# Performance work log

Hardware: AMD Instinct MI355X
Metric: run time of the kernel (lower is better)

## Reference

```python
import jax, jax.numpy as jnp
import numpy as np

B, T, C, H = 4, 4096, 1024, 64

def setup_inputs() -> dict:
    key = jax.random.key(0)
    k1, k2, k3, k4 = jax.random.split(key, 4)
    x = jax.random.normal(k1, (B, T, C), dtype=jnp.float32)
    # nn.Linear(C, H, bias=False): y = x @ W^T with W [H, C]; store as [C, H] for x @ W
    Wq = jax.random.normal(k2, (C, H), dtype=jnp.float32) * (C ** -0.5)
    Wk = jax.random.normal(k3, (C, H), dtype=jnp.float32) * (C ** -0.5)
    Wv = jax.random.normal(k4, (C, H), dtype=jnp.float32) * (C ** -0.5)
    return {"x": x, "Wq": Wq, "Wk": Wk, "Wv": Wv}

def reference(x, Wq, Wk, Wv):
    # Manual causal single-head attention (dropout p=0 -> identity).
    q = x @ Wq  # [B, T, H]
    k = x @ Wk  # [B, T, H]
    v = x @ Wv  # [B, T, H]
    scale = q.shape[-1] ** -0.5
    w = jnp.einsum('bth,bsh->bts', q, k) * scale  # [B, T, T] scores
    causal = jnp.tril(jnp.ones((x.shape[1], x.shape[1]), dtype=bool))
    w = jnp.where(causal, w, -jnp.inf)
    w = jax.nn.softmax(w, axis=-1)
    out = jnp.einsum('bts,bsh->bth', w, v)  # [B, T, H]
    return out
```

## Files before the change

### kernel.cpp

```cpp
#include <hip/hip_runtime.h>
#include <math.h>

#define Bn 4
#define Tn 4096
#define Cn 1024
#define Hn 64

typedef __attribute__((ext_vector_type(8))) short short8;
typedef __attribute__((ext_vector_type(4))) float floatx4;
typedef unsigned short ushort_t;

#define QSCALE 0.1803368801111204f

__device__ __forceinline__ ushort_t f2bf(float f) {
  union { float f; unsigned u; } v; v.f = f;
  unsigned r = v.u + 0x7FFFu + ((v.u >> 16) & 1u);
  return (ushort_t)(r >> 16);
}
__device__ __forceinline__ ushort_t f2bf_hu(float f) {
  union { float f; unsigned u; } v; v.f = f;
  return (ushort_t)((v.u + 0x8000u) >> 16);
}
__device__ __forceinline__ float bf2f(ushort_t h) {
  union { unsigned u; float f; } v; v.u = ((unsigned)h) << 16; return v.f;
}


__global__ __launch_bounds__(256) void wf_kernel(
    const float* __restrict__ Wq, const float* __restrict__ Wk,
    const float* __restrict__ Wv, ushort_t* __restrict__ Wf)
{
  __shared__ float ws[32][65];
  const int tid = threadIdx.x;
  const int m = blockIdx.x >> 5;
  const int g = blockIdx.x & 31;
  const float* W = (m == 0) ? Wq : (m == 1) ? Wk : Wv;
  const float4* src = (const float4*)(W + (size_t)g * 32 * Hn);
#pragma unroll
  for (int it = 0; it < 2; ++it) {
    int i4 = it * 256 + tid;
    float4 v = src[i4];
    int c = i4 >> 4, h = (i4 & 15) * 4;
    ws[c][h] = v.x; ws[c][h + 1] = v.y; ws[c][h + 2] = v.z; ws[c][h + 3] = v.w;
  }
  __syncthreads();
  const int nt = tid >> 6, lane = tid & 63;
  const int col = lane & 15, quad = lane >> 4;
  ushort_t t[8];
#pragma unroll
  for (int e = 0; e < 8; ++e) t[e] = f2bf(ws[quad * 8 + e][nt * 16 + col]);
  *(short8*)(Wf + ((size_t)((m * 32 + g) * 4 + nt) * 64 + lane) * 8) = *(short8*)t;
}

__global__ __launch_bounds__(256, 2) void qkv_proj_kernel(
    const float* __restrict__ x, const ushort_t* __restrict__ Wf,
    ushort_t* __restrict__ Qf, ushort_t* __restrict__ Kf,
    ushort_t* __restrict__ Vf)
{
  __shared__ __align__(16) char smem[67584];
  ushort_t* xs  = (ushort_t*)smem;
  ushort_t* red = (ushort_t*)smem;
  ushort_t* img = (ushort_t*)(smem + 49152);

  const int tid  = threadIdx.x;
  const int wv   = tid >> 6;
  const int lane = tid & 63;
  const int col  = lane & 15;
  const int quad = lane >> 4;
  const int blk  = blockIdx.x;
  const int row0 = blk * 32;

#pragma unroll
  for (int jj = 0; jj < 32; ++jj) {
    float4 v = *(const float4*)(x + (size_t)(row0 + jj) * Cn + wv * 256 + lane * 4);
    ushort4 u;
    u.x = f2bf(v.x); u.y = f2bf(v.y); u.z = f2bf(v.z); u.w = f2bf(v.w);
    *(ushort4*)(xs + (wv * 32 + jj) * 264 + lane * 4) = u;
  }

  floatx4 acc[2][3][4];
#pragma unroll
  for (int sub = 0; sub < 2; ++sub)
#pragma unroll
    for (int m = 0; m < 3; ++m)
#pragma unroll
      for (int nt = 0; nt < 4; ++nt) {
        acc[sub][m][nt][0] = 0.f; acc[sub][m][nt][1] = 0.f;
        acc[sub][m][nt][2] = 0.f; acc[sub][m][nt][3] = 0.f;
      }

#pragma unroll
  for (int ch = 0; ch < 8; ++ch) {
    const int gg = wv * 8 + ch;
    short8 af[2];
#pragma unroll
    for (int sub = 0; sub < 2; ++sub)
      af[sub] = *(const short8*)(xs + (wv * 32 + sub * 16 + col) * 264 + ch * 32 + quad * 8);
#pragma unroll
    for (int m = 0; m < 3; ++m)
#pragma unroll
      for (int nt = 0; nt < 4; ++nt) {
        short8 bf = *(const short8*)(Wf + ((size_t)((m * 32 + gg) * 4 + nt) * 64 + lane) * 8);
        acc[0][m][nt] = __builtin_amdgcn_mfma_f32_16x16x32_bf16(af[0], bf, acc[0][m][nt], 0, 0, 0);
        acc[1][m][nt] = __builtin_amdgcn_mfma_f32_16x16x32_bf16(af[1], bf, acc[1][m][nt], 0, 0, 0);
      }
  }
  __syncthreads();

#pragma unroll
  for (int sub = 0; sub < 2; ++sub)
#pragma unroll
    for (int m = 0; m < 3; ++m)
#pragma unroll
      for (int nt = 0; nt < 4; ++nt) {
        const int p = (sub * 3 + m) * 4 + nt;
        ushort4 u;
        u.x = f2bf(acc[sub][m][nt][0]); u.y = f2bf(acc[sub][m][nt][1]);
        u.z = f2bf(acc[sub][m][nt][2]); u.w = f2bf(acc[sub][m][nt][3]);
        *(ushort4*)&red[((p * 4 + wv) * 64 + lane) * 4] = u;
      }
  __syncthreads();

#pragma unroll
  for (int pp = 0; pp < 6; ++pp) {
    const int p = wv * 6 + pp;
    ushort4 w0 = *(const ushort4*)&red[((p * 4 + 0) * 64 + lane) * 4];
    ushort4 w1 = *(const ushort4*)&red[((p * 4 + 1) * 64 + lane) * 4];
    ushort4 w2 = *(const ushort4*)&red[((p * 4 + 2) * 64 + lane) * 4];
    ushort4 w3 = *(const ushort4*)&red[((p * 4 + 3) * 64 + lane) * 4];
    float v[4];
    v[0] = (bf2f(w0.x) + bf2f(w1.x)) + (bf2f(w2.x) + bf2f(w3.x));
    v[1] = (bf2f(w0.y) + bf2f(w1.y)) + (bf2f(w2.y) + bf2f(w3.y));
    v[2] = (bf2f(w0.z) + bf2f(w1.z)) + (bf2f(w2.z) + bf2f(w3.z));
    v[3] = (bf2f(w0.w) + bf2f(w1.w)) + (bf2f(w2.w) + bf2f(w3.w));
    const int sub = (p >= 12) ? 1 : 0;
    const int mrem = p - sub * 12;
    const int m = mrem >> 2, nt = mrem & 3;
#pragma unroll
    for (int r = 0; r < 4; ++r) {
      const int tlq = quad * 4 + r;
      if (m == 2) {
        img[4096 + nt * 512 + (quad * 16 + col) * 8 + sub * 4 + r] = f2bf(v[r]);
      } else {
        const int h = nt * 16 + col;
        const int idx = (h >> 5) * 512 + ((h >> 3) & 3) * 128 + tlq * 8 + (h & 7);
        img[m * 2048 + sub * 1024 + idx] = f2bf(m == 0 ? v[r] * QSCALE : v[r]);
      }
    }
  }
  __syncthreads();

  {
    const int b = blk >> 7, g = blk & 127;
#pragma unroll
    for (int sub = 0; sub < 2; ++sub) {
      const size_t qg = (size_t)(b * 256 + 2 * g + sub) * 1024 + tid * 4;
      *(uint2*)(Qf + qg) = *(const uint2*)&img[sub * 1024 + tid * 4];
      *(uint2*)(Kf + qg) = *(const uint2*)&img[2048 + sub * 1024 + tid * 4];
    }
    const int ht = tid >> 6;
    const size_t vg = ((size_t)(b * 64 + (g >> 1)) * 8 + ht * 2 + (g & 1)) * 512 + (tid & 63) * 8;
    *(short8*)(Vf + vg) = *(const short8*)&img[4096 + ht * 512 + (tid & 63) * 8];
  }
}

__global__ __launch_bounds__(256, 2) void attn_kernel(
    const ushort_t* __restrict__ Qf, const ushort_t* __restrict__ Kf,
    const ushort_t* __restrict__ Vf, float* __restrict__ out)
{
  __shared__ __align__(16) float Om[4][2][16][68];
  __shared__ __align__(16) float Ml[4][2][16];

  const int tid  = threadIdx.x;
  const int wv   = tid >> 6;
  const int lane = tid & 63;
  const int col  = lane & 15;
  const int quad = lane >> 4;
  const int b   = blockIdx.x & 3;
  const int idx = blockIdx.x >> 2;
  const int g   = (idx < 64) ? (127 - 2 * idx) : (2 * (idx - 64));

  short8 qf[2][2];
#pragma unroll
  for (int sub = 0; sub < 2; ++sub)
#pragma unroll
    for (int half = 0; half < 2; ++half)
      qf[sub][half] = *(const short8*)(Qf + (size_t)(b * 256 + 2 * g + sub) * 1024 + half * 512 + lane * 8);

  const ushort_t* Kbase = Kf + (size_t)b * 256 * 1024;
  const ushort_t* Vbase = Vf + (size_t)b * 64 * 8 * 512;

  short8 ones;
#pragma unroll
  for (int e = 0; e < 8; ++e) ones[e] = (short)0x3F80;

  floatx4 o[2][4], ol[2];
#pragma unroll
  for (int sub = 0; sub < 2; ++sub) {
#pragma unroll
    for (int ht = 0; ht < 4; ++ht) { o[sub][ht][0]=0.f; o[sub][ht][1]=0.f; o[sub][ht][2]=0.f; o[sub][ht][3]=0.f; }
    ol[sub][0]=0.f; ol[sub][1]=0.f; ol[sub][2]=0.f; ol[sub][3]=0.f;
  }

  const int ntile = ((g * 32 + 31) >> 6) + 1;
  const int dtile = ntile - 1;

  short8 kf[8], kfn[8];
#pragma unroll
  for (int kt = 0; kt < 4; ++kt) {
    const ushort_t* kp = Kbase + (size_t)wv * 4096 + kt * 1024 + lane * 8;
    kf[kt * 2]     = *(const short8*)(kp);
    kf[kt * 2 + 1] = *(const short8*)(kp + 512);
  }

  for (int i = wv; i < ntile; i += 4) {
    short8 vf[8];
#pragma unroll
    for (int ht = 0; ht < 4; ++ht) {
#pragma unroll
      for (int kh = 0; kh < 2; ++kh)
        vf[ht * 2 + kh] = *(const short8*)(Vbase + ((size_t)i * 8 + ht * 2 + kh) * 512 + lane * 8);
    }
#pragma unroll
    for (int kt = 0; kt < 4; ++kt) {
      const ushort_t* kp = Kbase + (size_t)(i + 4) * 4096 + kt * 1024 + lane * 8;
      kfn[kt * 2]     = *(const short8*)(kp);
      kfn[kt * 2 + 1] = *(const short8*)(kp + 512);
    }

    floatx4 s[2][4];
    __builtin_amdgcn_s_setprio(1);
#pragma unroll
    for (int sub = 0; sub < 2; ++sub)
#pragma unroll
      for (int kt = 0; kt < 4; ++kt) {
        floatx4 c; c[0]=0.f; c[1]=0.f; c[2]=0.f; c[3]=0.f;
        c = __builtin_amdgcn_mfma_f32_16x16x32_bf16(kf[kt * 2],     qf[sub][0], c, 0, 0, 0);
        c = __builtin_amdgcn_mfma_f32_16x16x32_bf16(kf[kt * 2 + 1], qf[sub][1], c, 0, 0, 0);
        s[sub][kt] = c;
      }
    __builtin_amdgcn_s_setprio(0);

    if (i == dtile) {
#pragma unroll
      for (int sub = 0; sub < 2; ++sub)
#pragma unroll
        for (int kt = 0; kt < 4; ++kt)
#pragma unroll
          for (int r = 0; r < 4; ++r)
            if (64 * i + kt * 16 + quad * 4 + r > g * 32 + sub * 16 + col)
              s[sub][kt][r] = -INFINITY;
    }

#pragma unroll
    for (int sub = 0; sub < 2; ++sub)
#pragma unroll
      for (int kt = 0; kt < 4; ++kt)
#pragma unroll
        for (int r = 0; r < 4; ++r)
          s[sub][kt][r] = __builtin_amdgcn_exp2f(s[sub][kt][r]);

    short8 pf[2][2];
#pragma unroll
    for (int sub = 0; sub < 2; ++sub)
#pragma unroll
      for (int kh = 0; kh < 2; ++kh) {
        ushort_t tmp[8];
#pragma unroll
        for (int half = 0; half < 2; ++half)
#pragma unroll
          for (int r = 0; r < 4; ++r)
            tmp[half * 4 + r] = f2bf_hu(s[sub][2 * kh + half][r]);
        pf[sub][kh] = *(short8*)tmp;
      }

    __builtin_amdgcn_s_setprio(1);
#pragma unroll
    for (int sub = 0; sub < 2; ++sub) {
#pragma unroll
      for (int ht = 0; ht < 4; ++ht) {
        o[sub][ht] = __builtin_amdgcn_mfma_f32_16x16x32_bf16(pf[sub][0], vf[ht * 2],     o[sub][ht], 0, 0, 0);
        o[sub][ht] = __builtin_amdgcn_mfma_f32_16x16x32_bf16(pf[sub][1], vf[ht * 2 + 1], o[sub][ht], 0, 0, 0);
      }
      ol[sub] = __builtin_amdgcn_mfma_f32_16x16x32_bf16(pf[sub][0], ones, ol[sub], 0, 0, 0);
      ol[sub] = __builtin_amdgcn_mfma_f32_16x16x32_bf16(pf[sub][1], ones, ol[sub], 0, 0, 0);
    }
    __builtin_amdgcn_s_setprio(0);

#pragma unroll
    for (int u2 = 0; u2 < 8; ++u2) kf[u2] = kfn[u2];
  }

#pragma unroll
  for (int sub = 0; sub < 2; ++sub) {
#pragma unroll
    for (int ht = 0; ht < 4; ++ht)
#pragma unroll
      for (int r = 0; r < 4; ++r)
        Om[wv][sub][quad * 4 + r][ht * 16 + col] = o[sub][ht][r];
    if (col == 0) {
#pragma unroll
      for (int r = 0; r < 4; ++r) Ml[wv][sub][quad * 4 + r] = ol[sub][r];
    }
  }
  __syncthreads();

  const int rr = tid >> 4, h4 = (tid & 15) * 4;
#pragma unroll
  for (int sub = 0; sub < 2; ++sub) {
    float L = (Ml[0][sub][rr] + Ml[1][sub][rr]) + (Ml[2][sub][rr] + Ml[3][sub][rr]);
    float4 a; a.x = 0.f; a.y = 0.f; a.z = 0.f; a.w = 0.f;
#pragma unroll
    for (int w = 0; w < 4; ++w) {
      float4 ov = *(const float4*)&Om[w][sub][rr][h4];
      a.x += ov.x; a.y += ov.y; a.z += ov.z; a.w += ov.w;
    }
    float inv = 1.f / L;
    a.x *= inv; a.y *= inv; a.z *= inv; a.w *= inv;
    *(float4*)(out + (size_t)(b * Tn + g * 32 + sub * 16 + rr) * Hn + h4) = a;
  }
}

extern "C" void kernel_launch(void* const* d_in, const int* in_sizes, int n_in,
                              void* d_out, int out_size, void* d_ws, size_t ws_size,
                              hipStream_t stream) {
  const float* x  = (const float*)d_in[0];
  const float* Wq = (const float*)d_in[1];
  const float* Wk = (const float*)d_in[2];
  const float* Wv = (const float*)d_in[3];
  float* out = (float*)d_out;

  ushort_t* Qf = (ushort_t*)d_ws;
  ushort_t* Kf = Qf + (size_t)Bn * Tn * Hn;
  ushort_t* Vf = Kf + (size_t)Bn * Tn * Hn;
  ushort_t* Wf = Vf + (size_t)Bn * Tn * Hn;

  wf_kernel<<<dim3(96), dim3(256), 0, stream>>>(Wq, Wk, Wv, Wf);
  qkv_proj_kernel<<<dim3(512), dim3(256), 0, stream>>>(x, Wf, Qf, Kf, Vf);
  attn_kernel<<<dim3(Bn * 128), dim3(256), 0, stream>>>(Qf, Kf, Vf, out);
}
```

Baseline: 124.0 us.

## Double-buffer weight and K/V register loads to overlap memory with MFMA

In the QKV projection, weight fragments are now prefetched into two alternating register buffers one chunk ahead of the MFMAs that consume them, and the x loads are batched 16 rows at a time before conversion. In the attention loop, both K and V tiles are prefetched one iteration ahead using ping-pong register sets, so V is no longer loaded just before use. The intent is to hide global load latency behind matrix work. The cost is higher register pressure (24 extra short8 in projection, 32 in attention), which could lower occupancy or cause spills.

```diff
diff --git a/kernel.cpp b/kernel.cpp
--- a/kernel.cpp
+++ b/kernel.cpp
@@ -70,12 +70,30 @@
   const int blk  = blockIdx.x;
   const int row0 = blk * 32;
 
-#pragma unroll
-  for (int jj = 0; jj < 32; ++jj) {
-    float4 v = *(const float4*)(x + (size_t)(row0 + jj) * Cn + wv * 256 + lane * 4);
-    ushort4 u;
-    u.x = f2bf(v.x); u.y = f2bf(v.y); u.z = f2bf(v.z); u.w = f2bf(v.w);
-    *(ushort4*)(xs + (wv * 32 + jj) * 264 + lane * 4) = u;
+#define BF_LOAD(DST, GG)                                                        \
+  do {                                                                          \
+    _Pragma("unroll")                                                           \
+    for (int k = 0; k < 12; ++k) {                                              \
+      const int m_ = k >> 2, nt_ = k & 3;                                       \
+      DST[k] = *(const short8*)(Wf + ((size_t)((m_ * 32 + (GG)) * 4 + nt_) * 64 + lane) * 8); \
+    }                                                                           \
+  } while (0)
+
+  short8 bfA[12], bfB[12];
+  BF_LOAD(bfA, wv * 8);
+
+#pragma unroll
+  for (int half = 0; half < 2; ++half) {
+    float4 v[16];
+#pragma unroll
+    for (int jj = 0; jj < 16; ++jj)
+      v[jj] = *(const float4*)(x + (size_t)(row0 + half * 16 + jj) * Cn + wv * 256 + lane * 4);
+#pragma unroll
+    for (int jj = 0; jj < 16; ++jj) {
+      ushort4 u;
+      u.x = f2bf(v[jj].x); u.y = f2bf(v[jj].y); u.z = f2bf(v[jj].z); u.w = f2bf(v[jj].w);
+      *(ushort4*)(xs + (wv * 32 + half * 16 + jj) * 264 + lane * 4) = u;
+    }
   }
 
   floatx4 acc[2][3][4];
@@ -89,21 +107,25 @@
         acc[sub][m][nt][2] = 0.f; acc[sub][m][nt][3] = 0.f;
       }
 
-#pragma unroll
-  for (int ch = 0; ch < 8; ++ch) {
-    const int gg = wv * 8 + ch;
-    short8 af[2];
-#pragma unroll
-    for (int sub = 0; sub < 2; ++sub)
-      af[sub] = *(const short8*)(xs + (wv * 32 + sub * 16 + col) * 264 + ch * 32 + quad * 8);
-#pragma unroll
-    for (int m = 0; m < 3; ++m)
-#pragma unroll
-      for (int nt = 0; nt < 4; ++nt) {
-        short8 bf = *(const short8*)(Wf + ((size_t)((m * 32 + gg) * 4 + nt) * 64 + lane) * 8);
-        acc[0][m][nt] = __builtin_amdgcn_mfma_f32_16x16x32_bf16(af[0], bf, acc[0][m][nt], 0, 0, 0);
-        acc[1][m][nt] = __builtin_amdgcn_mfma_f32_16x16x32_bf16(af[1], bf, acc[1][m][nt], 0, 0, 0);
-      }
+#define QKV_MFMA(BF, CH)                                                        \
+  do {                                                                          \
+    short8 af0 = *(const short8*)(xs + (wv * 32 + col) * 264 + (CH) * 32 + quad * 8);        \
+    short8 af1 = *(const short8*)(xs + (wv * 32 + 16 + col) * 264 + (CH) * 32 + quad * 8);   \
+    _Pragma("unroll")                                                           \
+    for (int k = 0; k < 12; ++k) {                                              \
+      const int m_ = k >> 2, nt_ = k & 3;                                       \
+      acc[0][m_][nt_] = __builtin_amdgcn_mfma_f32_16x16x32_bf16(af0, BF[k], acc[0][m_][nt_], 0, 0, 0); \
+      acc[1][m_][nt_] = __builtin_amdgcn_mfma_f32_16x16x32_bf16(af1, BF[k], acc[1][m_][nt_], 0, 0, 0); \
+    }                                                                           \
+  } while (0)
+
+#pragma unroll
+  for (int ch2 = 0; ch2 < 4; ++ch2) {
+    const int ch = ch2 * 2;
+    BF_LOAD(bfB, wv * 8 + ch + 1);
+    QKV_MFMA(bfA, ch);
+    if (ch2 < 3) BF_LOAD(bfA, wv * 8 + ch + 2);
+    QKV_MFMA(bfB, ch + 1);
   }
   __syncthreads();
 
@@ -205,90 +227,96 @@
   const int ntile = ((g * 32 + 31) >> 6) + 1;
   const int dtile = ntile - 1;
 
-  short8 kf[8], kfn[8];
-#pragma unroll
-  for (int kt = 0; kt < 4; ++kt) {
-    const ushort_t* kp = Kbase + (size_t)wv * 4096 + kt * 1024 + lane * 8;
-    kf[kt * 2]     = *(const short8*)(kp);
-    kf[kt * 2 + 1] = *(const short8*)(kp + 512);
-  }
-
-  for (int i = wv; i < ntile; i += 4) {
-    short8 vf[8];
-#pragma unroll
-    for (int ht = 0; ht < 4; ++ht) {
-#pragma unroll
-      for (int kh = 0; kh < 2; ++kh)
-        vf[ht * 2 + kh] = *(const short8*)(Vbase + ((size_t)i * 8 + ht * 2 + kh) * 512 + lane * 8);
-    }
-#pragma unroll
-    for (int kt = 0; kt < 4; ++kt) {
-      const ushort_t* kp = Kbase + (size_t)(i + 4) * 4096 + kt * 1024 + lane * 8;
-      kfn[kt * 2]     = *(const short8*)(kp);
-      kfn[kt * 2 + 1] = *(const short8*)(kp + 512);
-    }
-
-    floatx4 s[2][4];
-    __builtin_amdgcn_s_setprio(1);
-#pragma unroll
-    for (int sub = 0; sub < 2; ++sub)
-#pragma unroll
-      for (int kt = 0; kt < 4; ++kt) {
-        floatx4 c; c[0]=0.f; c[1]=0.f; c[2]=0.f; c[3]=0.f;
-        c = __builtin_amdgcn_mfma_f32_16x16x32_bf16(kf[kt * 2],     qf[sub][0], c, 0, 0, 0);
-        c = __builtin_amdgcn_mfma_f32_16x16x32_bf16(kf[kt * 2 + 1], qf[sub][1], c, 0, 0, 0);
-        s[sub][kt] = c;
-      }
-    __builtin_amdgcn_s_setprio(0);
-
-    if (i == dtile) {
-#pragma unroll
-      for (int sub = 0; sub < 2; ++sub)
-#pragma unroll
-        for (int kt = 0; kt < 4; ++kt)
-#pragma unroll
-          for (int r = 0; r < 4; ++r)
-            if (64 * i + kt * 16 + quad * 4 + r > g * 32 + sub * 16 + col)
-              s[sub][kt][r] = -INFINITY;
-    }
-
-#pragma unroll
-    for (int sub = 0; sub < 2; ++sub)
-#pragma unroll
-      for (int kt = 0; kt < 4; ++kt)
-#pragma unroll
-        for (int r = 0; r < 4; ++r)
-          s[sub][kt][r] = __builtin_amdgcn_exp2f(s[sub][kt][r]);
-
-    short8 pf[2][2];
-#pragma unroll
-    for (int sub = 0; sub < 2; ++sub)
-#pragma unroll
-      for (int kh = 0; kh < 2; ++kh) {
-        ushort_t tmp[8];
-#pragma unroll
-        for (int half = 0; half < 2; ++half)
-#pragma unroll
-          for (int r = 0; r < 4; ++r)
-            tmp[half * 4 + r] = f2bf_hu(s[sub][2 * kh + half][r]);
-        pf[sub][kh] = *(short8*)tmp;
-      }
-
-    __builtin_amdgcn_s_setprio(1);
-#pragma unroll
-    for (int sub = 0; sub < 2; ++sub) {
-#pragma unroll
-      for (int ht = 0; ht < 4; ++ht) {
-        o[sub][ht] = __builtin_amdgcn_mfma_f32_16x16x32_bf16(pf[sub][0], vf[ht * 2],     o[sub][ht], 0, 0, 0);
-        o[sub][ht] = __builtin_amdgcn_mfma_f32_16x16x32_bf16(pf[sub][1], vf[ht * 2 + 1], o[sub][ht], 0, 0, 0);
-      }
-      ol[sub] = __builtin_amdgcn_mfma_f32_16x16x32_bf16(pf[sub][0], ones, ol[sub], 0, 0, 0);
-      ol[sub] = __builtin_amdgcn_mfma_f32_16x16x32_bf16(pf[sub][1], ones, ol[sub], 0, 0, 0);
-    }
-    __builtin_amdgcn_s_setprio(0);
-
-#pragma unroll
-    for (int u2 = 0; u2 < 8; ++u2) kf[u2] = kfn[u2];
+  short8 kfA[8], vfA[8], kfB[8], vfB[8];
+
+#define LOADKV(KF, VF, II)                                                      \
+  do {                                                                          \
+    _Pragma("unroll")                                                           \
+    for (int kt = 0; kt < 4; ++kt) {                                            \
+      const ushort_t* kp = Kbase + (size_t)(II) * 4096 + kt * 1024 + lane * 8;  \
+      KF[kt * 2]     = *(const short8*)(kp);                                    \
+      KF[kt * 2 + 1] = *(const short8*)(kp + 512);                              \
+    }                                                                           \
+    _Pragma("unroll")                                                           \
+    for (int ht = 0; ht < 4; ++ht) {                                            \
+      _Pragma("unroll")                                                         \
+      for (int kh = 0; kh < 2; ++kh)                                            \
+        VF[ht * 2 + kh] = *(const short8*)(Vbase + ((size_t)(II) * 8 + ht * 2 + kh) * 512 + lane * 8); \
+    }                                                                           \
+  } while (0)
+
+#define TILE_BODY(KF, VF, II)                                                   \
+  do {                                                                          \
+    floatx4 s[2][4];                                                            \
+    __builtin_amdgcn_s_setprio(1);                                              \
+    _Pragma("unroll")                                                           \
+    for (int sub = 0; sub < 2; ++sub)                                           \
+      _Pragma("unroll")                                                         \
+      for (int kt = 0; kt < 4; ++kt) {                                          \
+        floatx4 c; c[0]=0.f; c[1]=0.f; c[2]=0.f; c[3]=0.f;                      \
+        c = __builtin_amdgcn_mfma_f32_16x16x32_bf16(KF[kt * 2],     qf[sub][0], c, 0, 0, 0); \
+        c = __builtin_amdgcn_mfma_f32_16x16x32_bf16(KF[kt * 2 + 1], qf[sub][1], c, 0, 0, 0); \
+        s[sub][kt] = c;                                                         \
+      }                                                                         \
+    __builtin_amdgcn_s_setprio(0);                                              \
+    if ((II) == dtile) {                                                        \
+      _Pragma("unroll")                                                         \
+      for (int sub = 0; sub < 2; ++sub)                                         \
+        _Pragma("unroll")                                                       \
+        for (int kt = 0; kt < 4; ++kt)                                          \
+          _Pragma("unroll")                                                     \
+          for (int r = 0; r < 4; ++r)                                           \
+            if (64 * (II) + kt * 16 + quad * 4 + r > g * 32 + sub * 16 + col)   \
+              s[sub][kt][r] = -INFINITY;                                        \
+    }                                                                           \
+    _Pragma("unroll")                                                           \
+    for (int sub = 0; sub < 2; ++sub)                                           \
+      _Pragma("unroll")                                                         \
+      for (int kt = 0; kt < 4; ++kt)                                            \
+        _Pragma("unroll")                                                       \
+        for (int r = 0; r < 4; ++r)                                             \
+          s[sub][kt][r] = __builtin_amdgcn_exp2f(s[sub][kt][r]);                \
+    short8 pf[2][2];                                                            \
+    _Pragma("unroll")                                                           \
+    for (int sub = 0; sub < 2; ++sub)                                           \
+      _Pragma("unroll")                                                         \
+      for (int kh = 0; kh < 2; ++kh) {                                          \
+        ushort_t tmp[8];                                                        \
+        _Pragma("unroll")                                                       \
+        for (int half = 0; half < 2; ++half)                                    \
+          _Pragma("unroll")                                                     \
+          for (int r = 0; r < 4; ++r)                                           \
+            tmp[half * 4 + r] = f2bf_hu(s[sub][2 * kh + half][r]);              \
+        pf[sub][kh] = *(short8*)tmp;                                            \
+      }                                                                         \
+    __builtin_amdgcn_s_setprio(1);                                              \
+    _Pragma("unroll")                                                           \
+    for (int sub = 0; sub < 2; ++sub) {                                         \
+      _Pragma("unroll")                                                         \
+      for (int ht = 0; ht < 4; ++ht) {                                          \
+        o[sub][ht] = __builtin_amdgcn_mfma_f32_16x16x32_bf16(pf[sub][0], VF[ht * 2],     o[sub][ht], 0, 0, 0); \
+        o[sub][ht] = __builtin_amdgcn_mfma_f32_16x16x32_bf16(pf[sub][1], VF[ht * 2 + 1], o[sub][ht], 0, 0, 0); \
+      }                                                                         \
+      ol[sub] = __builtin_amdgcn_mfma_f32_16x16x32_bf16(pf[sub][0], ones, ol[sub], 0, 0, 0); \
+      ol[sub] = __builtin_amdgcn_mfma_f32_16x16x32_bf16(pf[sub][1], ones, ol[sub], 0, 0, 0); \
+    }                                                                           \
+    __builtin_amdgcn_s_setprio(0);                                              \
+  } while (0)
+
+  {
+    int i = wv;
+    if (i < ntile) LOADKV(kfA, vfA, i);
+    while (i < ntile) {
+      int j = i + 4;
+      if (j < ntile) LOADKV(kfB, vfB, j);
+      TILE_BODY(kfA, vfA, i);
+      i = j;
+      if (i >= ntile) break;
+      j = i + 4;
+      if (j < ntile) LOADKV(kfA, vfA, j);
+      TILE_BODY(kfB, vfB, i);
+      i = j;
+    }
   }
 
 #pragma unroll
```

After: 129.6 us. 4.5% more time.

## Halve rows per block in projection and attention kernels to double grid size

Applied to the files above, without the earlier changes.

Both the QKV projection and attention kernels now process 16 query rows per block instead of 32, doubling the grid to 1024 blocks each and raising launch bounds to 4 blocks per CU, with shared memory halved to match. The attention loop drops the software-prefetched next K tile and loads K inside each iteration. The projection preloads all 12 weight fragments per chunk before its MFMAs. The aim is more parallelism and occupancy on the many-CU GPU. The cost is that each K/V tile is reloaded twice as often, Wf weights are streamed by twice as many blocks, and the K prefetch overlap is lost.

```diff
diff --git a/kernel.cpp b/kernel.cpp
--- a/kernel.cpp
+++ b/kernel.cpp
@@ -52,15 +52,15 @@
   *(short8*)(Wf + ((size_t)((m * 32 + g) * 4 + nt) * 64 + lane) * 8) = *(short8*)t;
 }
 
-__global__ __launch_bounds__(256, 2) void qkv_proj_kernel(
+__global__ __launch_bounds__(256, 4) void qkv_proj_kernel(
     const float* __restrict__ x, const ushort_t* __restrict__ Wf,
     ushort_t* __restrict__ Qf, ushort_t* __restrict__ Kf,
     ushort_t* __restrict__ Vf)
 {
-  __shared__ __align__(16) char smem[67584];
+  __shared__ __align__(16) char smem[33792];
   ushort_t* xs  = (ushort_t*)smem;
   ushort_t* red = (ushort_t*)smem;
-  ushort_t* img = (ushort_t*)(smem + 49152);
+  ushort_t* img = (ushort_t*)(smem + 24576);
 
   const int tid  = threadIdx.x;
   const int wv   = tid >> 6;
@@ -68,62 +68,62 @@
   const int col  = lane & 15;
   const int quad = lane >> 4;
   const int blk  = blockIdx.x;
-  const int row0 = blk * 32;
-
-#pragma unroll
-  for (int jj = 0; jj < 32; ++jj) {
-    float4 v = *(const float4*)(x + (size_t)(row0 + jj) * Cn + wv * 256 + lane * 4);
-    ushort4 u;
-    u.x = f2bf(v.x); u.y = f2bf(v.y); u.z = f2bf(v.z); u.w = f2bf(v.w);
-    *(ushort4*)(xs + (wv * 32 + jj) * 264 + lane * 4) = u;
-  }
-
-  floatx4 acc[2][3][4];
-#pragma unroll
-  for (int sub = 0; sub < 2; ++sub)
-#pragma unroll
-    for (int m = 0; m < 3; ++m)
-#pragma unroll
-      for (int nt = 0; nt < 4; ++nt) {
-        acc[sub][m][nt][0] = 0.f; acc[sub][m][nt][1] = 0.f;
-        acc[sub][m][nt][2] = 0.f; acc[sub][m][nt][3] = 0.f;
-      }
+  const int row0 = blk * 16;
+
+#pragma unroll
+  for (int hb = 0; hb < 2; ++hb) {
+    float4 v[8];
+#pragma unroll
+    for (int jj = 0; jj < 8; ++jj)
+      v[jj] = *(const float4*)(x + (size_t)(row0 + hb * 8 + jj) * Cn + wv * 256 + lane * 4);
+#pragma unroll
+    for (int jj = 0; jj < 8; ++jj) {
+      ushort4 u;
+      u.x = f2bf(v[jj].x); u.y = f2bf(v[jj].y); u.z = f2bf(v[jj].z); u.w = f2bf(v[jj].w);
+      *(ushort4*)(xs + (wv * 16 + hb * 8 + jj) * 264 + lane * 4) = u;
+    }
+  }
+
+  floatx4 acc[3][4];
+#pragma unroll
+  for (int m = 0; m < 3; ++m)
+#pragma unroll
+    for (int nt = 0; nt < 4; ++nt) {
+      acc[m][nt][0] = 0.f; acc[m][nt][1] = 0.f;
+      acc[m][nt][2] = 0.f; acc[m][nt][3] = 0.f;
+    }
 
 #pragma unroll
   for (int ch = 0; ch < 8; ++ch) {
     const int gg = wv * 8 + ch;
-    short8 af[2];
-#pragma unroll
-    for (int sub = 0; sub < 2; ++sub)
-      af[sub] = *(const short8*)(xs + (wv * 32 + sub * 16 + col) * 264 + ch * 32 + quad * 8);
-#pragma unroll
-    for (int m = 0; m < 3; ++m)
-#pragma unroll
-      for (int nt = 0; nt < 4; ++nt) {
-        short8 bf = *(const short8*)(Wf + ((size_t)((m * 32 + gg) * 4 + nt) * 64 + lane) * 8);
-        acc[0][m][nt] = __builtin_amdgcn_mfma_f32_16x16x32_bf16(af[0], bf, acc[0][m][nt], 0, 0, 0);
-        acc[1][m][nt] = __builtin_amdgcn_mfma_f32_16x16x32_bf16(af[1], bf, acc[1][m][nt], 0, 0, 0);
-      }
-  }
-  __syncthreads();
-
-#pragma unroll
-  for (int sub = 0; sub < 2; ++sub)
-#pragma unroll
-    for (int m = 0; m < 3; ++m)
-#pragma unroll
-      for (int nt = 0; nt < 4; ++nt) {
-        const int p = (sub * 3 + m) * 4 + nt;
-        ushort4 u;
-        u.x = f2bf(acc[sub][m][nt][0]); u.y = f2bf(acc[sub][m][nt][1]);
-        u.z = f2bf(acc[sub][m][nt][2]); u.w = f2bf(acc[sub][m][nt][3]);
-        *(ushort4*)&red[((p * 4 + wv) * 64 + lane) * 4] = u;
-      }
-  __syncthreads();
-
-#pragma unroll
-  for (int pp = 0; pp < 6; ++pp) {
-    const int p = wv * 6 + pp;
+    short8 bf[12];
+#pragma unroll
+    for (int k = 0; k < 12; ++k) {
+      const int m_ = k >> 2, nt_ = k & 3;
+      bf[k] = *(const short8*)(Wf + ((size_t)((m_ * 32 + gg) * 4 + nt_) * 64 + lane) * 8);
+    }
+    short8 af = *(const short8*)(xs + (wv * 16 + col) * 264 + ch * 32 + quad * 8);
+#pragma unroll
+    for (int k = 0; k < 12; ++k)
+      acc[k >> 2][k & 3] = __builtin_amdgcn_mfma_f32_16x16x32_bf16(af, bf[k], acc[k >> 2][k & 3], 0, 0, 0);
+  }
+  __syncthreads();
+
+#pragma unroll
+  for (int m = 0; m < 3; ++m)
+#pragma unroll
+    for (int nt = 0; nt < 4; ++nt) {
+      const int p = m * 4 + nt;
+      ushort4 u;
+      u.x = f2bf(acc[m][nt][0]); u.y = f2bf(acc[m][nt][1]);
+      u.z = f2bf(acc[m][nt][2]); u.w = f2bf(acc[m][nt][3]);
+      *(ushort4*)&red[((p * 4 + wv) * 64 + lane) * 4] = u;
+    }
+  __syncthreads();
+
+#pragma unroll
+  for (int pp = 0; pp < 3; ++pp) {
+    const int p = wv * 3 + pp;
     ushort4 w0 = *(const ushort4*)&red[((p * 4 + 0) * 64 + lane) * 4];
     ushort4 w1 = *(const ushort4*)&red[((p * 4 + 1) * 64 + lane) * 4];
     ushort4 w2 = *(const ushort4*)&red[((p * 4 + 2) * 64 + lane) * 4];
@@ -133,43 +133,39 @@
     v[1] = (bf2f(w0.y) + bf2f(w1.y)) + (bf2f(w2.y) + bf2f(w3.y));
     v[2] = (bf2f(w0.z) + bf2f(w1.z)) + (bf2f(w2.z) + bf2f(w3.z));
     v[3] = (bf2f(w0.w) + bf2f(w1.w)) + (bf2f(w2.w) + bf2f(w3.w));
-    const int sub = (p >= 12) ? 1 : 0;
-    const int mrem = p - sub * 12;
-    const int m = mrem >> 2, nt = mrem & 3;
+    const int m = p >> 2, nt = p & 3;
 #pragma unroll
     for (int r = 0; r < 4; ++r) {
       const int tlq = quad * 4 + r;
       if (m == 2) {
-        img[4096 + nt * 512 + (quad * 16 + col) * 8 + sub * 4 + r] = f2bf(v[r]);
+        img[2048 + nt * 256 + (quad * 16 + col) * 4 + r] = f2bf(v[r]);
       } else {
         const int h = nt * 16 + col;
         const int idx = (h >> 5) * 512 + ((h >> 3) & 3) * 128 + tlq * 8 + (h & 7);
-        img[m * 2048 + sub * 1024 + idx] = f2bf(m == 0 ? v[r] * QSCALE : v[r]);
+        img[m * 1024 + idx] = f2bf(m == 0 ? v[r] * QSCALE : v[r]);
       }
     }
   }
   __syncthreads();
 
   {
-    const int b = blk >> 7, g = blk & 127;
-#pragma unroll
-    for (int sub = 0; sub < 2; ++sub) {
-      const size_t qg = (size_t)(b * 256 + 2 * g + sub) * 1024 + tid * 4;
-      *(uint2*)(Qf + qg) = *(const uint2*)&img[sub * 1024 + tid * 4];
-      *(uint2*)(Kf + qg) = *(const uint2*)&img[2048 + sub * 1024 + tid * 4];
-    }
+    const int b = blk >> 8, g = blk & 255;
+    const size_t qg = (size_t)(b * 256 + g) * 1024 + tid * 4;
+    *(uint2*)(Qf + qg) = *(const uint2*)&img[tid * 4];
+    *(uint2*)(Kf + qg) = *(const uint2*)&img[1024 + tid * 4];
     const int ht = tid >> 6;
-    const size_t vg = ((size_t)(b * 64 + (g >> 1)) * 8 + ht * 2 + (g & 1)) * 512 + (tid & 63) * 8;
-    *(short8*)(Vf + vg) = *(const short8*)&img[4096 + ht * 512 + (tid & 63) * 8];
-  }
-}
-
-__global__ __launch_bounds__(256, 2) void attn_kernel(
+    const size_t vg = ((size_t)(b * 64 + (g >> 2)) * 8 + ht * 2 + ((g >> 1) & 1)) * 512
+                      + (tid & 63) * 8 + (g & 1) * 4;
+    *(uint2*)(Vf + vg) = *(const uint2*)&img[2048 + ht * 256 + (tid & 63) * 4];
+  }
+}
+
+__global__ __launch_bounds__(256, 4) void attn_kernel(
     const ushort_t* __restrict__ Qf, const ushort_t* __restrict__ Kf,
     const ushort_t* __restrict__ Vf, float* __restrict__ out)
 {
-  __shared__ __align__(16) float Om[4][2][16][68];
-  __shared__ __align__(16) float Ml[4][2][16];
+  __shared__ __align__(16) float Om[4][16][68];
+  __shared__ __align__(16) float Ml[4][16];
 
   const int tid  = threadIdx.x;
   const int wv   = tid >> 6;
@@ -178,14 +174,12 @@
   const int quad = lane >> 4;
   const int b   = blockIdx.x & 3;
   const int idx = blockIdx.x >> 2;
-  const int g   = (idx < 64) ? (127 - 2 * idx) : (2 * (idx - 64));
-
-  short8 qf[2][2];
-#pragma unroll
-  for (int sub = 0; sub < 2; ++sub)
-#pragma unroll
-    for (int half = 0; half < 2; ++half)
-      qf[sub][half] = *(const short8*)(Qf + (size_t)(b * 256 + 2 * g + sub) * 1024 + half * 512 + lane * 8);
+  const int g   = (idx < 128) ? (255 - 2 * idx) : (2 * (idx - 128));
+
+  short8 qf[2];
+#pragma unroll
+  for (int half = 0; half < 2; ++half)
+    qf[half] = *(const short8*)(Qf + (size_t)(b * 256 + g) * 1024 + half * 512 + lane * 8);
 
   const ushort_t* Kbase = Kf + (size_t)b * 256 * 1024;
   const ushort_t* Vbase = Vf + (size_t)b * 64 * 8 * 512;
@@ -194,130 +188,101 @@
 #pragma unroll
   for (int e = 0; e < 8; ++e) ones[e] = (short)0x3F80;
 
-  floatx4 o[2][4], ol[2];
-#pragma unroll
-  for (int sub = 0; sub < 2; ++sub) {
-#pragma unroll
-    for (int ht = 0; ht < 4; ++ht) { o[sub][ht][0]=0.f; o[sub][ht][1]=0.f; o[sub][ht][2]=0.f; o[sub][ht][3]=0.f; }
-    ol[sub][0]=0.f; ol[sub][1]=0.f; ol[sub][2]=0.f; ol[sub][3]=0.f;
-  }
-
-  const int ntile = ((g * 32 + 31) >> 6) + 1;
+  floatx4 o[4], ol;
+#pragma unroll
+  for (int ht = 0; ht < 4; ++ht) { o[ht][0]=0.f; o[ht][1]=0.f; o[ht][2]=0.f; o[ht][3]=0.f; }
+  ol[0]=0.f; ol[1]=0.f; ol[2]=0.f; ol[3]=0.f;
+
+  const int ntile = (g >> 2) + 1;
   const int dtile = ntile - 1;
 
-  short8 kf[8], kfn[8];
-#pragma unroll
-  for (int kt = 0; kt < 4; ++kt) {
-    const ushort_t* kp = Kbase + (size_t)wv * 4096 + kt * 1024 + lane * 8;
-    kf[kt * 2]     = *(const short8*)(kp);
-    kf[kt * 2 + 1] = *(const short8*)(kp + 512);
-  }
-
   for (int i = wv; i < ntile; i += 4) {
-    short8 vf[8];
+    short8 kf[8], vf[8];
+#pragma unroll
+    for (int kt = 0; kt < 4; ++kt) {
+      const ushort_t* kp = Kbase + (size_t)i * 4096 + kt * 1024 + lane * 8;
+      kf[kt * 2]     = *(const short8*)(kp);
+      kf[kt * 2 + 1] = *(const short8*)(kp + 512);
+    }
 #pragma unroll
     for (int ht = 0; ht < 4; ++ht) {
 #pragma unroll
       for (int kh = 0; kh < 2; ++kh)
         vf[ht * 2 + kh] = *(const short8*)(Vbase + ((size_t)i * 8 + ht * 2 + kh) * 512 + lane * 8);
     }
+
+    floatx4 s[4];
+    __builtin_amdgcn_s_setprio(1);
 #pragma unroll
     for (int kt = 0; kt < 4; ++kt) {
-      const ushort_t* kp = Kbase + (size_t)(i + 4) * 4096 + kt * 1024 + lane * 8;
-      kfn[kt * 2]     = *(const short8*)(kp);
-      kfn[kt * 2 + 1] = *(const short8*)(kp + 512);
-    }
-
-    floatx4 s[2][4];
+      floatx4 c; c[0]=0.f; c[1]=0.f; c[2]=0.f; c[3]=0.f;
+      c = __builtin_amdgcn_mfma_f32_16x16x32_bf16(kf[kt * 2],     qf[0], c, 0, 0, 0);
+      c = __builtin_amdgcn_mfma_f32_16x16x32_bf16(kf[kt * 2 + 1], qf[1], c, 0, 0, 0);
+      s[kt] = c;
+    }
+    __builtin_amdgcn_s_setprio(0);
+
+    if (i == dtile) {
+#pragma unroll
+      for (int kt = 0; kt < 4; ++kt)
+#pragma unroll
+        for (int r = 0; r < 4; ++r)
+          if (64 * i + kt * 16 + quad * 4 + r > g * 16 + col)
+            s[kt][r] = -INFINITY;
+    }
+
+#pragma unroll
+    for (int kt = 0; kt < 4; ++kt)
+#pragma unroll
+      for (int r = 0; r < 4; ++r)
+        s[kt][r] = __builtin_amdgcn_exp2f(s[kt][r]);
+
+    short8 pf[2];
+#pragma unroll
+    for (int kh = 0; kh < 2; ++kh) {
+      ushort_t tmp[8];
+#pragma unroll
+      for (int half = 0; half < 2; ++half)
+#pragma unroll
+        for (int r = 0; r < 4; ++r)
+          tmp[half * 4 + r] = f2bf_hu(s[2 * kh + half][r]);
+      pf[kh] = *(short8*)tmp;
+    }
+
     __builtin_amdgcn_s_setprio(1);
 #pragma unroll
-    for (int sub = 0; sub < 2; ++sub)
-#pragma unroll
-      for (int kt = 0; kt < 4; ++kt) {
-        floatx4 c; c[0]=0.f; c[1]=0.f; c[2]=0.f; c[3]=0.f;
-        c = __builtin_amdgcn_mfma_f32_16x16x32_bf16(kf[kt * 2],     qf[sub][0], c, 0, 0, 0);
-        c = __builtin_amdgcn_mfma_f32_16x16x32_bf16(kf[kt * 2 + 1], qf[sub][1], c, 0, 0, 0);
-        s[sub][kt] = c;
-      }
+    for (int ht = 0; ht < 4; ++ht) {
+      o[ht] = __builtin_amdgcn_mfma_f32_16x16x32_bf16(pf[0], vf[ht * 2],     o[ht], 0, 0, 0);
+      o[ht] = __builtin_amdgcn_mfma_f32_16x16x32_bf16(pf[1], vf[ht * 2 + 1], o[ht], 0, 0, 0);
+    }
+    ol = __builtin_amdgcn_mfma_f32_16x16x32_bf16(pf[0], ones, ol, 0, 0, 0);
+    ol = __builtin_amdgcn_mfma_f32_16x16x32_bf16(pf[1], ones, ol, 0, 0, 0);
     __builtin_amdgcn_s_setprio(0);
-
-    if (i == dtile) {
-#pragma unroll
-      for (int sub = 0; sub < 2; ++sub)
-#pragma unroll
-        for (int kt = 0; kt < 4; ++kt)
-#pragma unroll
-          for (int r = 0; r < 4; ++r)
-            if (64 * i + kt * 16 + quad * 4 + r > g * 32 + sub * 16 + col)
-              s[sub][kt][r] = -INFINITY;
-    }
-
-#pragma unroll
-    for (int sub = 0; sub < 2; ++sub)
-#pragma unroll
-      for (int kt = 0; kt < 4; ++kt)
-#pragma unroll
-        for (int r = 0; r < 4; ++r)
-          s[sub][kt][r] = __builtin_amdgcn_exp2f(s[sub][kt][r]);
-
-    short8 pf[2][2];
-#pragma unroll
-    for (int sub = 0; sub < 2; ++sub)
-#pragma unroll
-      for (int kh = 0; kh < 2; ++kh) {
-        ushort_t tmp[8];
-#pragma unroll
-        for (int half = 0; half < 2; ++half)
-#pragma unroll
-          for (int r = 0; r < 4; ++r)
-            tmp[half * 4 + r] = f2bf_hu(s[sub][2 * kh + half][r]);
-        pf[sub][kh] = *(short8*)tmp;
-      }
-
-    __builtin_amdgcn_s_setprio(1);
-#pragma unroll
-    for (int sub = 0; sub < 2; ++sub) {
-#pragma unroll
-      for (int ht = 0; ht < 4; ++ht) {
-        o[sub][ht] = __builtin_amdgcn_mfma_f32_16x16x32_bf16(pf[sub][0], vf[ht * 2],     o[sub][ht], 0, 0, 0);
-        o[sub][ht] = __builtin_amdgcn_mfma_f32_16x16x32_bf16(pf[sub][1], vf[ht * 2 + 1], o[sub][ht], 0, 0, 0);
-      }
-      ol[sub] = __builtin_amdgcn_mfma_f32_16x16x32_bf16(pf[sub][0], ones, ol[sub], 0, 0, 0);
-      ol[sub] = __builtin_amdgcn_mfma_f32_16x16x32_bf16(pf[sub][1], ones, ol[sub], 0, 0, 0);
-    }
-    __builtin_amdgcn_s_setprio(0);
-
-#pragma unroll
-    for (int u2 = 0; u2 < 8; ++u2) kf[u2] = kfn[u2];
-  }
-
-#pragma unroll
-  for (int sub = 0; sub < 2; ++sub) {
-#pragma unroll
-    for (int ht = 0; ht < 4; ++ht)
-#pragma unroll
-      for (int r = 0; r < 4; ++r)
-        Om[wv][sub][quad * 4 + r][ht * 16 + col] = o[sub][ht][r];
-    if (col == 0) {
-#pragma unroll
-      for (int r = 0; r < 4; ++r) Ml[wv][sub][quad * 4 + r] = ol[sub][r];
-    }
+  }
+
+#pragma unroll
+  for (int ht = 0; ht < 4; ++ht)
+#pragma unroll
+    for (int r = 0; r < 4; ++r)
+      Om[wv][quad * 4 + r][ht * 16 + col] = o[ht][r];
+  if (col == 0) {
+#pragma unroll
+    for (int r = 0; r < 4; ++r) Ml[wv][quad * 4 + r] = ol[r];
   }
   __syncthreads();
 
   const int rr = tid >> 4, h4 = (tid & 15) * 4;
-#pragma unroll
-  for (int sub = 0; sub < 2; ++sub) {
-    float L = (Ml[0][sub][rr] + Ml[1][sub][rr]) + (Ml[2][sub][rr] + Ml[3][sub][rr]);
+  {
+    float L = (Ml[0][rr] + Ml[1][rr]) + (Ml[2][rr] + Ml[3][rr]);
     float4 a; a.x = 0.f; a.y = 0.f; a.z = 0.f; a.w = 0.f;
 #pragma unroll
     for (int w = 0; w < 4; ++w) {
-      float4 ov = *(const float4*)&Om[w][sub][rr][h4];
+      float4 ov = *(const float4*)&Om[w][rr][h4];
       a.x += ov.x; a.y += ov.y; a.z += ov.z; a.w += ov.w;
     }
     float inv = 1.f / L;
     a.x *= inv; a.y *= inv; a.z *= inv; a.w *= inv;
-    *(float4*)(out + (size_t)(b * Tn + g * 32 + sub * 16 + rr) * Hn + h4) = a;
+    *(float4*)(out + (size_t)(b * Tn + g * 16 + rr) * Hn + h4) = a;
   }
 }
 
@@ -336,6 +301,6 @@
   ushort_t* Wf = Vf + (size_t)Bn * Tn * Hn;
 
   wf_kernel<<<dim3(96), dim3(256), 0, stream>>>(Wq, Wk, Wv, Wf);
-  qkv_proj_kernel<<<dim3(512), dim3(256), 0, stream>>>(x, Wf, Qf, Kf, Vf);
-  attn_kernel<<<dim3(Bn * 128), dim3(256), 0, stream>>>(Qf, Kf, Vf, out);
-}
+  qkv_proj_kernel<<<dim3(1024), dim3(256), 0, stream>>>(x, Wf, Qf, Kf, Vf);
+  attn_kernel<<<dim3(Bn * 256), dim3(256), 0, stream>>>(Qf, Kf, Vf, out);
+}
```

After: 130.7 us. +5.4%, slower.

## Batch global loads ahead of compute with compiler fences, drop K prefetch

Applied to the files above, without the earlier changes.

Regroups loads so that all global reads for a step are issued together before the compute. The x-to-bf16 conversion loads 16 rows at once, the projection loads all 12 weight fragments before its MFMAs, and an empty asm memory fence keeps the compiler from interleaving. In the attention loop the double-buffered K prefetch of the next tile is replaced by loading K and V at the start of each iteration. The aim is more memory-level parallelism and less register pressure, at the cost of no longer hiding K load latency across iterations.

```diff
diff --git a/kernel.cpp b/kernel.cpp
--- a/kernel.cpp
+++ b/kernel.cpp
@@ -11,6 +11,8 @@
 typedef unsigned short ushort_t;
 
 #define QSCALE 0.1803368801111204f
+
+#define ILP_FENCE() asm volatile("" ::: "memory")
 
 __device__ __forceinline__ ushort_t f2bf(float f) {
   union { float f; unsigned u; } v; v.f = f;
@@ -71,11 +73,18 @@
   const int row0 = blk * 32;
 
 #pragma unroll
-  for (int jj = 0; jj < 32; ++jj) {
-    float4 v = *(const float4*)(x + (size_t)(row0 + jj) * Cn + wv * 256 + lane * 4);
-    ushort4 u;
-    u.x = f2bf(v.x); u.y = f2bf(v.y); u.z = f2bf(v.z); u.w = f2bf(v.w);
-    *(ushort4*)(xs + (wv * 32 + jj) * 264 + lane * 4) = u;
+  for (int half = 0; half < 2; ++half) {
+    float4 v[16];
+#pragma unroll
+    for (int jj = 0; jj < 16; ++jj)
+      v[jj] = *(const float4*)(x + (size_t)(row0 + half * 16 + jj) * Cn + wv * 256 + lane * 4);
+    ILP_FENCE();
+#pragma unroll
+    for (int jj = 0; jj < 16; ++jj) {
+      ushort4 u;
+      u.x = f2bf(v[jj].x); u.y = f2bf(v[jj].y); u.z = f2bf(v[jj].z); u.w = f2bf(v[jj].w);
+      *(ushort4*)(xs + (wv * 32 + half * 16 + jj) * 264 + lane * 4) = u;
+    }
   }
 
   floatx4 acc[2][3][4];
@@ -92,18 +101,21 @@
 #pragma unroll
   for (int ch = 0; ch < 8; ++ch) {
     const int gg = wv * 8 + ch;
-    short8 af[2];
-#pragma unroll
-    for (int sub = 0; sub < 2; ++sub)
-      af[sub] = *(const short8*)(xs + (wv * 32 + sub * 16 + col) * 264 + ch * 32 + quad * 8);
-#pragma unroll
-    for (int m = 0; m < 3; ++m)
-#pragma unroll
-      for (int nt = 0; nt < 4; ++nt) {
-        short8 bf = *(const short8*)(Wf + ((size_t)((m * 32 + gg) * 4 + nt) * 64 + lane) * 8);
-        acc[0][m][nt] = __builtin_amdgcn_mfma_f32_16x16x32_bf16(af[0], bf, acc[0][m][nt], 0, 0, 0);
-        acc[1][m][nt] = __builtin_amdgcn_mfma_f32_16x16x32_bf16(af[1], bf, acc[1][m][nt], 0, 0, 0);
-      }
+    short8 bf[12];
+#pragma unroll
+    for (int k = 0; k < 12; ++k) {
+      const int m_ = k >> 2, nt_ = k & 3;
+      bf[k] = *(const short8*)(Wf + ((size_t)((m_ * 32 + gg) * 4 + nt_) * 64 + lane) * 8);
+    }
+    short8 af0 = *(const short8*)(xs + (wv * 32 + col) * 264 + ch * 32 + quad * 8);
+    short8 af1 = *(const short8*)(xs + (wv * 32 + 16 + col) * 264 + ch * 32 + quad * 8);
+    ILP_FENCE();
+#pragma unroll
+    for (int k = 0; k < 12; ++k) {
+      const int m_ = k >> 2, nt_ = k & 3;
+      acc[0][m_][nt_] = __builtin_amdgcn_mfma_f32_16x16x32_bf16(af0, bf[k], acc[0][m_][nt_], 0, 0, 0);
+      acc[1][m_][nt_] = __builtin_amdgcn_mfma_f32_16x16x32_bf16(af1, bf[k], acc[1][m_][nt_], 0, 0, 0);
+    }
   }
   __syncthreads();
 
@@ -205,28 +217,21 @@
   const int ntile = ((g * 32 + 31) >> 6) + 1;
   const int dtile = ntile - 1;
 
-  short8 kf[8], kfn[8];
-#pragma unroll
-  for (int kt = 0; kt < 4; ++kt) {
-    const ushort_t* kp = Kbase + (size_t)wv * 4096 + kt * 1024 + lane * 8;
-    kf[kt * 2]     = *(const short8*)(kp);
-    kf[kt * 2 + 1] = *(const short8*)(kp + 512);
-  }
-
   for (int i = wv; i < ntile; i += 4) {
-    short8 vf[8];
+    short8 kf[8], vf[8];
+#pragma unroll
+    for (int kt = 0; kt < 4; ++kt) {
+      const ushort_t* kp = Kbase + (size_t)i * 4096 + kt * 1024 + lane * 8;
+      kf[kt * 2]     = *(const short8*)(kp);
+      kf[kt * 2 + 1] = *(const short8*)(kp + 512);
+    }
 #pragma unroll
     for (int ht = 0; ht < 4; ++ht) {
 #pragma unroll
       for (int kh = 0; kh < 2; ++kh)
         vf[ht * 2 + kh] = *(const short8*)(Vbase + ((size_t)i * 8 + ht * 2 + kh) * 512 + lane * 8);
     }
-#pragma unroll
-    for (int kt = 0; kt < 4; ++kt) {
-      const ushort_t* kp = Kbase + (size_t)(i + 4) * 4096 + kt * 1024 + lane * 8;
-      kfn[kt * 2]     = *(const short8*)(kp);
-      kfn[kt * 2 + 1] = *(const short8*)(kp + 512);
-    }
+    ILP_FENCE();
 
     floatx4 s[2][4];
     __builtin_amdgcn_s_setprio(1);
@@ -286,9 +291,6 @@
       ol[sub] = __builtin_amdgcn_mfma_f32_16x16x32_bf16(pf[sub][1], ones, ol[sub], 0, 0, 0);
     }
     __builtin_amdgcn_s_setprio(0);
-
-#pragma unroll
-    for (int u2 = 0; u2 < 8; ++u2) kf[u2] = kfn[u2];
   }
 
 #pragma unroll
```

Result: no change. 123.3 us, median of 2 (-0.6%).
